# Kernel optimization log

Hardware: AMD Instinct MI355X
Metric: run time of the kernel (lower is better)

Reference implementation:

```python
import jax, jax.numpy as jnp
import numpy as np

D = 128   # node feature dim
C = 2     # classes
N = 50000 # nodes
E = 500000  # edges (before self-loops)
H1 = 2    # conv1 heads
NEG_SLOPE = 0.2
BN_EPS = 1e-5


def setup_inputs() -> dict:
    key = jax.random.key(0)
    ks = jax.random.split(key, 24)
    rn = lambda k, shape, s=0.05: jax.random.normal(k, shape, dtype=jnp.float32) * s
    inp = {
        'x': jax.random.normal(ks[0], (N, D), dtype=jnp.float32),
        'edge_index': jax.random.randint(ks[1], (2, E), 0, N, dtype=jnp.int64),
        # conv1: GATConv(D, D, heads=2, concat=True)
        'W1': rn(ks[2], (D, H1 * D)),
        'att_src1': rn(ks[3], (H1, D)),
        'att_dst1': rn(ks[4], (H1, D)),
        'bias1': jnp.zeros((H1 * D,), jnp.float32),
        # conv2: GATConv(2D, D, heads=1, concat=False)
        'W2': rn(ks[5], (2 * D, D)),
        'att_src2': rn(ks[6], (1, D)),
        'att_dst2': rn(ks[7], (1, D)),
        'bias2': jnp.zeros((D,), jnp.float32),
        # lin1 = MLP([3D, 96]) : Linear -> ReLU -> BatchNorm1d
        'Wl': rn(ks[8], (3 * D, 96)), 'bl': jnp.zeros((96,), jnp.float32),
        'gl': jnp.ones((96,), jnp.float32), 'betal': jnp.zeros((96,), jnp.float32),
        # mlp1 = MLP([96, 96, C]) : two (Linear -> ReLU -> BN) blocks
        'Wa': rn(ks[9], (96, 96)), 'ba': jnp.zeros((96,), jnp.float32),
        'ga': jnp.ones((96,), jnp.float32), 'betaa': jnp.zeros((96,), jnp.float32),
        'Wb': rn(ks[10], (96, C)), 'bb': jnp.zeros((C,), jnp.float32),
        'gb': jnp.ones((C,), jnp.float32), 'betab': jnp.zeros((C,), jnp.float32),
    }
    return inp


def gat_conv(x, src, dst, W, att_src, att_dst, bias, heads, out_dim, concat):
    # PyG GATConv: h = x W -> [N,H,F]; per-edge logit leakyrelu(a_s.h_src + a_d.h_dst);
    # segment softmax over edges grouped by destination; weighted scatter-sum.
    n = x.shape[0]
    h = (x @ W).reshape(n, heads, out_dim)
    a_src = jnp.einsum('nhd,hd->nh', h, att_src)  # [N,H]
    a_dst = jnp.einsum('nhd,hd->nh', h, att_dst)
    alpha = jax.nn.leaky_relu(a_src[src] + a_dst[dst], NEG_SLOPE)  # [Etot,H]
    m = jax.ops.segment_max(alpha, dst, num_segments=n)            # [N,H]
    e = jnp.exp(alpha - m[dst])
    s = jax.ops.segment_sum(e, dst, num_segments=n)
    w = e / (s[dst] + 1e-16)                                       # [Etot,H]
    out = jax.ops.segment_sum(h[src] * w[:, :, None], dst, num_segments=n)  # [N,H,F]
    out = out.reshape(n, heads * out_dim) if concat else out.mean(axis=1)
    return out + bias


def mlp_block(x, W, b, gamma, beta):
    # Linear -> ReLU -> BatchNorm1d (training-mode batch stats, biased var)
    y = jax.nn.relu(x @ W + b)
    mu = y.mean(axis=0)
    var = ((y - mu) ** 2).mean(axis=0)
    return gamma * (y - mu) / jnp.sqrt(var + BN_EPS) + beta


def reference(x, edge_index, W1, att_src1, att_dst1, bias1,
              W2, att_src2, att_dst2, bias2,
              Wl, bl, gl, betal, Wa, ba, ga, betaa, Wb, bb, gb, betab):
    n = x.shape[0]
    # PyG GATConv default add_self_loops=True
    loops = jnp.arange(n, dtype=edge_index.dtype)
    src = jnp.concatenate([edge_index[0], loops])
    dst = jnp.concatenate([edge_index[1], loops])
    x1 = gat_conv(x, src, dst, W1, att_src1, att_dst1, bias1, H1, D, True)    # [N,2D]
    x2 = gat_conv(x1, src, dst, W2, att_src2, att_dst2, bias2, 1, D, False)   # [N,D]
    h = jnp.concatenate([x1, x2], axis=1)                                      # [N,3D]
    h = mlp_block(h, Wl, bl, gl, betal)     # lin1
    h = mlp_block(h, Wa, ba, ga, betaa)     # mlp1 layer 1
    h = mlp_block(h, Wb, bb, gb, betab)     # mlp1 layer 2
    return h
```

## Files before the change

### kernel.cpp

```cpp
#include <hip/hip_runtime.h>
#include <hip/hip_bf16.h>
#include <cstdint>
#include <cstddef>

#define NNODES 50000
#define NEDGES 500000
#define ETOT   (NEDGES + NNODES)
#define MAXDEG 96

typedef __attribute__((ext_vector_type(8))) short short8;
typedef __attribute__((ext_vector_type(8))) unsigned short ushort8v;
typedef __attribute__((ext_vector_type(4))) float floatx4;
typedef __attribute__((ext_vector_type(4))) unsigned short ushort4v;

__device__ __forceinline__ unsigned short f2bf(float f) {
    union { __hip_bfloat16 h; unsigned short u; } cv;
    cv.h = __float2bfloat16(f);
    return cv.u;
}
__device__ __forceinline__ float bf2f(unsigned short u) {
    union { unsigned int i; float f; } cv;
    cv.i = ((unsigned int)u) << 16;
    return cv.f;
}

#define GBM 128
#define GBN 64
#define GBK 32

__global__ __launch_bounds__(256, 4) void gemm_mfma(
    const unsigned short* __restrict__ A, int lda,
    const unsigned short* __restrict__ Bt,
    float* __restrict__ C,
    unsigned short* __restrict__ Cb,
    const float* __restrict__ bias,
    float* __restrict__ colsum, float* __restrict__ colsq,
    const float* __restrict__ att_s, const float* __restrict__ att_d,
    float* __restrict__ as_out, float* __restrict__ ad_out, int Hheads,
    int M, int N, int K, int do_relu)
{
    __shared__ __attribute__((aligned(16))) unsigned short Alds[GBM * GBK];
    __shared__ __attribute__((aligned(16))) unsigned short Blds[GBN * GBK];
    __shared__ float scol[GBN], sqcol[GBN];

    int tid = threadIdx.x;
    int wave = tid >> 6, lane = tid & 63;
    int row0 = blockIdx.y * GBM;
    int col0 = blockIdx.x * GBN;
    int m = lane & 15, q = lane >> 4;

    floatx4 acc[2][4] = {};

    for (int k0 = 0; k0 < K; k0 += GBK) {
        #pragma unroll
        for (int i = 0; i < 2; ++i) {
            int c = tid + i * 256;
            int r = c >> 2, off = (c & 3) * 8;
            int gr = row0 + r;
            short8 v = {};
            if (gr < M) v = *(const short8*)(A + (size_t)gr * lda + k0 + off);
            *(short8*)(Alds + r * GBK + off) = v;
        }
        {
            int r = tid >> 2, off = (tid & 3) * 8;
            short8 v = *(const short8*)(Bt + (size_t)(col0 + r) * K + k0 + off);
            *(short8*)(Blds + r * GBK + off) = v;
        }
        __syncthreads();

        short8 a0 = *(const short8*)(Alds + (wave * 32 + m) * GBK + q * 8);
        short8 a1 = *(const short8*)(Alds + (wave * 32 + 16 + m) * GBK + q * 8);
        #pragma unroll
        for (int ct = 0; ct < 4; ++ct) {
            short8 b = *(const short8*)(Blds + (ct * 16 + m) * GBK + q * 8);
            acc[0][ct] = __builtin_amdgcn_mfma_f32_16x16x32_bf16(a0, b, acc[0][ct], 0, 0, 0);
            acc[1][ct] = __builtin_amdgcn_mfma_f32_16x16x32_bf16(a1, b, acc[1][ct], 0, 0, 0);
        }
        __syncthreads();
    }

    float ps[4] = {}, pq[4] = {};
    #pragma unroll
    for (int rt = 0; rt < 2; ++rt) {
        #pragma unroll
        for (int r = 0; r < 4; ++r) {
            int gr = row0 + wave * 32 + rt * 16 + q * 4 + r;
            float ds = 0.f, dd = 0.f;
            #pragma unroll
            for (int ct = 0; ct < 4; ++ct) {
                int gc = col0 + ct * 16 + m;
                float v = acc[rt][ct][r];
                if (gc < N) {
                    if (att_s != nullptr) { ds += v * att_s[gc]; dd += v * att_d[gc]; }
                    float vb = v;
                    if (bias != nullptr) vb += bias[gc];
                    if (do_relu) vb = fmaxf(vb, 0.f);
                    if (gr < M) {
                        if (C  != nullptr) C[(size_t)gr * N + gc] = vb;
                        if (Cb != nullptr) Cb[(size_t)gr * N + gc] = f2bf(vb);
                        ps[ct] += vb; pq[ct] += vb * vb;
                    }
                }
            }
            if (att_s != nullptr) {
                #pragma unroll
                for (int off = 1; off < 16; off <<= 1) {
                    ds += __shfl_xor(ds, off);
                    dd += __shfl_xor(dd, off);
                }
                if (m == 0 && gr < M) {
                    int head = col0 >> 7;
                    atomicAdd(&as_out[gr * Hheads + head], ds);
                    atomicAdd(&ad_out[gr * Hheads + head], dd);
                }
            }
        }
    }
    if (colsum != nullptr) {
        if (tid < GBN) { scol[tid] = 0.f; sqcol[tid] = 0.f; }
        __syncthreads();
        #pragma unroll
        for (int ct = 0; ct < 4; ++ct) {
            atomicAdd(&scol[ct * 16 + m], ps[ct]);
            atomicAdd(&sqcol[ct * 16 + m], pq[ct]);
        }
        __syncthreads();
        if (tid < GBN) {
            int gc = col0 + tid;
            if (gc < N) {
                atomicAdd(&colsum[gc], scol[tid]);
                atomicAdd(&colsq[gc], sqcol[tid]);
            }
        }
    }
}

__global__ void cast_x_k(const float* __restrict__ x, unsigned short* __restrict__ xb, int total4) {
    int i = blockIdx.x * blockDim.x + threadIdx.x;
    if (i >= total4) return;
    const float4 v = ((const float4*)x)[i];
    ushort4v o;
    o.x = f2bf(v.x); o.y = f2bf(v.y); o.z = f2bf(v.z); o.w = f2bf(v.w);
    ((ushort4v*)xb)[i] = o;
}

__global__ void cast_weights(const float* __restrict__ W1, const float* __restrict__ W2,
                             const float* __restrict__ Wl,
                             unsigned short* __restrict__ W1t, unsigned short* __restrict__ W2t,
                             unsigned short* __restrict__ Wlt) {
    int i = blockIdx.x * 256 + threadIdx.x;
    if (i < 32768) {
        int n = i >> 7, k = i & 127;
        W1t[i] = f2bf(W1[k * 256 + n]);
    } else if (i < 65536) {
        int j = i - 32768;
        int n = j >> 8, k = j & 255;
        W2t[j] = f2bf(W2[k * 128 + n]);
    } else if (i < 114688) {
        int j = i - 65536;
        int n = j / 384, k = j % 384;
        Wlt[j] = (n < 96) ? f2bf(Wl[(size_t)k * 96 + n]) : (unsigned short)0;
    }
}

__global__ void bnfold_a(const float* __restrict__ csum, const float* __restrict__ csq,
                         const float* __restrict__ gamma, const float* __restrict__ beta,
                         const float* __restrict__ Wa, const float* __restrict__ ba,
                         unsigned short* __restrict__ Wat2, float* __restrict__ ba_f) {
    __shared__ float scl[96], shf[96];
    int tid = threadIdx.x;
    if (tid < 96) {
        float mu  = csum[tid] / (float)NNODES;
        float var = csq[tid] / (float)NNODES - mu * mu;
        if (var < 0.f) var = 0.f;
        float sc = gamma[tid] * rsqrtf(var + 1e-5f);
        scl[tid] = sc; shf[tid] = beta[tid] - mu * sc;
    }
    __syncthreads();
    for (int idx = tid; idx < 128 * 96; idx += 256) {
        int n = idx / 96, k = idx % 96;
        Wat2[idx] = (n < 96) ? f2bf(scl[k] * Wa[k * 96 + n]) : (unsigned short)0;
    }
    if (tid < 96) {
        float s = ba[tid];
        for (int k = 0; k < 96; ++k) s += shf[k] * Wa[k * 96 + tid];
        ba_f[tid] = s;
    }
}

__global__ void bnfold_b(const float* __restrict__ csum, const float* __restrict__ csq,
                         const float* __restrict__ gamma, const float* __restrict__ beta,
                         const float* __restrict__ Wb, const float* __restrict__ bb,
                         unsigned short* __restrict__ Wbt, float* __restrict__ bb_f) {
    __shared__ float scl[96], shf[96];
    int tid = threadIdx.x;
    if (tid < 96) {
        float mu  = csum[tid] / (float)NNODES;
        float var = csq[tid] / (float)NNODES - mu * mu;
        if (var < 0.f) var = 0.f;
        float sc = gamma[tid] * rsqrtf(var + 1e-5f);
        scl[tid] = sc; shf[tid] = beta[tid] - mu * sc;
    }
    __syncthreads();
    for (int idx = tid; idx < 64 * 96; idx += 256) {
        int n = idx / 96, k = idx % 96;
        Wbt[idx] = (n < 2) ? f2bf(scl[k] * Wb[k * 2 + n]) : (unsigned short)0;
    }
    if (tid < 2) {
        float s = bb[tid];
        for (int k = 0; k < 96; ++k) s += shf[k] * Wb[k * 2 + tid];
        bb_f[tid] = s;
    }
}

__global__ void bn_fin_apply(const float* __restrict__ csum, const float* __restrict__ csq,
                             const float* __restrict__ gamma, const float* __restrict__ beta,
                             float* __restrict__ y, int total) {
    int i = blockIdx.x * blockDim.x + threadIdx.x;
    if (i >= total) return;
    int j = i & 1;
    float mu  = csum[j] / (float)NNODES;
    float var = csq[j] / (float)NNODES - mu * mu;
    if (var < 0.f) var = 0.f;
    float sc = gamma[j] * rsqrtf(var + 1e-5f);
    float sh = beta[j] - mu * sc;
    y[i] = y[i] * sc + sh;
}

__device__ __forceinline__ void edge_src_dst(const int* ei, int e, int& src, int& dst) {
    if (e < NEDGES) { src = ei[e]; dst = ei[NEDGES + e]; }
    else { src = e - NEDGES; dst = src; }
}

__global__ __launch_bounds__(256) void csr_count(const int* __restrict__ ei, int* __restrict__ cnt) {
    int e = blockIdx.x * blockDim.x + threadIdx.x;
    if (e >= ETOT) return;
    int src, dst; edge_src_dst(ei, e, src, dst); (void)src;
    atomicAdd(&cnt[dst], 1);
}

#define SCAN_CH 1024
#define SCAN_NB ((NNODES + SCAN_CH - 1) / SCAN_CH)

__global__ __launch_bounds__(256) void scan1(const int* __restrict__ cnt, int* __restrict__ part) {
    int t = threadIdx.x;
    int base = blockIdx.x * SCAN_CH + t * 4;
    int4 v = {0, 0, 0, 0};
    if (base + 3 < NNODES) v = *(const int4*)(cnt + base);
    else {
        if (base + 0 < NNODES) v.x = cnt[base + 0];
        if (base + 1 < NNODES) v.y = cnt[base + 1];
        if (base + 2 < NNODES) v.z = cnt[base + 2];
        if (base + 3 < NNODES) v.w = cnt[base + 3];
    }
    int s = v.x + v.y + v.z + v.w;
    __shared__ int sm[256];
    sm[t] = s;
    __syncthreads();
    for (int off = 128; off > 0; off >>= 1) {
        if (t < off) sm[t] += sm[t + off];
        __syncthreads();
    }
    if (t == 0) part[blockIdx.x] = sm[0];
}

__global__ void scan2(int* __restrict__ part, int* __restrict__ rowstart) {
    int lane = threadIdx.x;
    int v = (lane < SCAN_NB) ? part[lane] : 0;
    #pragma unroll
    for (int off = 1; off < 64; off <<= 1) {
        int t = __shfl_up(v, off);
        if (lane >= off) v += t;
    }
    int ex = __shfl_up(v, 1);
    if (lane == 0) ex = 0;
    if (lane < SCAN_NB) part[lane] = ex;
    if (lane == 0) rowstart[NNODES] = ETOT;
}

__global__ __launch_bounds__(256) void scan3(const int* __restrict__ cnt, const int* __restrict__ part,
                                             int* __restrict__ rowstart, int* __restrict__ cursor) {
    int t = threadIdx.x;
    int base = blockIdx.x * SCAN_CH + t * 4;
    int4 v = {0, 0, 0, 0};
    if (base + 3 < NNODES) v = *(const int4*)(cnt + base);
    else {
        if (base + 0 < NNODES) v.x = cnt[base + 0];
        if (base + 1 < NNODES) v.y = cnt[base + 1];
        if (base + 2 < NNODES) v.z = cnt[base + 2];
        if (base + 3 < NNODES) v.w = cnt[base + 3];
    }
    int s = v.x + v.y + v.z + v.w;
    __shared__ int sm[2][256];
    sm[0][t] = s;
    __syncthreads();
    int cur = 0;
    #pragma unroll
    for (int off = 1; off < 256; off <<= 1) {
        int nxt = cur ^ 1;
        int val = sm[cur][t];
        if (t >= off) val += sm[cur][t - off];
        sm[nxt][t] = val;
        __syncthreads();
        cur = nxt;
    }
    int p = sm[cur][t] - s + part[blockIdx.x];
    if (base + 0 < NNODES) { rowstart[base + 0] = p; cursor[base + 0] = p; } p += v.x;
    if (base + 1 < NNODES) { rowstart[base + 1] = p; cursor[base + 1] = p; } p += v.y;
    if (base + 2 < NNODES) { rowstart[base + 2] = p; cursor[base + 2] = p; } p += v.z;
    if (base + 3 < NNODES) { rowstart[base + 3] = p; cursor[base + 3] = p; }
}

__global__ __launch_bounds__(256) void csr_fill(const int* __restrict__ ei,
                                                int* __restrict__ cursor,
                                                int* __restrict__ esrc) {
    int e = blockIdx.x * blockDim.x + threadIdx.x;
    if (e >= ETOT) return;
    int src, dst; edge_src_dst(ei, e, src, dst);
    int pos = atomicAdd(&cursor[dst], 1);
    esrc[pos] = src;
}

__global__ __launch_bounds__(256) void gat_gather_h2(
    const int* __restrict__ rowstart, const int* __restrict__ esrc,
    const unsigned short* __restrict__ hb, const float* __restrict__ a_src,
    const float* __restrict__ a_dst, const float* __restrict__ bias,
    unsigned short* __restrict__ xcat)
{
    __shared__ float wl[4][2][MAXDEG];
    __shared__ int   esl[4][MAXDEG];
    int wave = threadIdx.x >> 6;
    int n = (blockIdx.x * blockDim.x + threadIdx.x) >> 6;
    int lane = threadIdx.x & 63;
    if (n >= NNODES) return;
    int beg = rowstart[n], end = rowstart[n + 1];
    int deg = end - beg;
    float ad0 = a_dst[n * 2], ad1 = a_dst[n * 2 + 1];

    float m0 = -1e30f, m1 = -1e30f;
    for (int idx = lane; idx < deg; idx += 64) {
        int s = esrc[beg + idx];
        float l0 = a_src[s * 2] + ad0;     l0 = l0 >= 0.f ? l0 : 0.2f * l0;
        float l1 = a_src[s * 2 + 1] + ad1; l1 = l1 >= 0.f ? l1 : 0.2f * l1;
        m0 = fmaxf(m0, l0); m1 = fmaxf(m1, l1);
        if (idx < MAXDEG) { wl[wave][0][idx] = l0; wl[wave][1][idx] = l1; esl[wave][idx] = s; }
    }
    #pragma unroll
    for (int off = 1; off < 64; off <<= 1) {
        m0 = fmaxf(m0, __shfl_xor(m0, off));
        m1 = fmaxf(m1, __shfl_xor(m1, off));
    }
    float s0 = 0.f, s1 = 0.f;
    for (int idx = lane; idx < deg; idx += 64) {
        float l0, l1;
        if (idx < MAXDEG) { l0 = wl[wave][0][idx]; l1 = wl[wave][1][idx]; }
        else {
            int s = esrc[beg + idx];
            l0 = a_src[s * 2] + ad0;     l0 = l0 >= 0.f ? l0 : 0.2f * l0;
            l1 = a_src[s * 2 + 1] + ad1; l1 = l1 >= 0.f ? l1 : 0.2f * l1;
        }
        float e0 = __expf(l0 - m0), e1 = __expf(l1 - m1);
        s0 += e0; s1 += e1;
        if (idx < MAXDEG) { wl[wave][0][idx] = e0; wl[wave][1][idx] = e1; }
    }
    #pragma unroll
    for (int off = 1; off < 64; off <<= 1) {
        s0 += __shfl_xor(s0, off);
        s1 += __shfl_xor(s1, off);
    }

    int g  = lane >> 5;
    int sl = lane & 31;
    int head = sl >> 4;
    float mh   = head ? m1 : m0;
    float invh = head ? 1.f / (s1 + 1e-16f) : 1.f / (s0 + 1e-16f);
    float adh  = head ? ad1 : ad0;

    float acc[8] = {}, acc2[8] = {};
    for (int idx = g; idx < deg; idx += 4) {
        int sA; float wA;
        if (idx < MAXDEG) { sA = esl[wave][idx]; wA = wl[wave][head][idx] * invh; }
        else {
            sA = esrc[beg + idx];
            float l = a_src[sA * 2 + head] + adh; l = l >= 0.f ? l : 0.2f * l;
            wA = __expf(l - mh) * invh;
        }
        const ushort8v hvA = *(const ushort8v*)(hb + (size_t)sA * 256 + sl * 8);
        int i2 = idx + 2;
        if (i2 < deg) {
            int sB; float wB;
            if (i2 < MAXDEG) { sB = esl[wave][i2]; wB = wl[wave][head][i2] * invh; }
            else {
                sB = esrc[beg + i2];
                float l = a_src[sB * 2 + head] + adh; l = l >= 0.f ? l : 0.2f * l;
                wB = __expf(l - mh) * invh;
            }
            const ushort8v hvB = *(const ushort8v*)(hb + (size_t)sB * 256 + sl * 8);
            #pragma unroll
            for (int j = 0; j < 8; ++j) acc2[j] += wB * bf2f(hvB[j]);
        }
        #pragma unroll
        for (int j = 0; j < 8; ++j) acc[j] += wA * bf2f(hvA[j]);
    }
    #pragma unroll
    for (int j = 0; j < 8; ++j) acc[j] += acc2[j];
    #pragma unroll
    for (int j = 0; j < 8; ++j) acc[j] += __shfl_xor(acc[j], 32);
    if (g == 0) {
        ushort8v o;
        #pragma unroll
        for (int j = 0; j < 8; ++j) o[j] = f2bf(acc[j] + bias[sl * 8 + j]);
        *(ushort8v*)(xcat + (size_t)n * 384 + sl * 8) = o;
    }
}

__global__ __launch_bounds__(256) void gat_gather_h1(
    const int* __restrict__ rowstart, const int* __restrict__ esrc,
    const unsigned short* __restrict__ hb, const float* __restrict__ a_src,
    const float* __restrict__ a_dst, const float* __restrict__ bias,
    unsigned short* __restrict__ xcat)
{
    __shared__ float wl[4][MAXDEG];
    __shared__ int   esl[4][MAXDEG];
    int wave = threadIdx.x >> 6;
    int n = (blockIdx.x * blockDim.x + threadIdx.x) >> 6;
    int lane = threadIdx.x & 63;
    if (n >= NNODES) return;
    int beg = rowstart[n], end = rowstart[n + 1];
    int deg = end - beg;
    float ad0 = a_dst[n];

    float m0 = -1e30f;
    for (int idx = lane; idx < deg; idx += 64) {
        int s = esrc[beg + idx];
        float l0 = a_src[s] + ad0; l0 = l0 >= 0.f ? l0 : 0.2f * l0;
        m0 = fmaxf(m0, l0);
        if (idx < MAXDEG) { wl[wave][idx] = l0; esl[wave][idx] = s; }
    }
    #pragma unroll
    for (int off = 1; off < 64; off <<= 1) m0 = fmaxf(m0, __shfl_xor(m0, off));
    float s0 = 0.f;
    for (int idx = lane; idx < deg; idx += 64) {
        float l0;
        if (idx < MAXDEG) l0 = wl[wave][idx];
        else {
            int s = esrc[beg + idx];
            l0 = a_src[s] + ad0; l0 = l0 >= 0.f ? l0 : 0.2f * l0;
        }
        float e0 = __expf(l0 - m0);
        s0 += e0;
        if (idx < MAXDEG) wl[wave][idx] = e0;
    }
    #pragma unroll
    for (int off = 1; off < 64; off <<= 1) s0 += __shfl_xor(s0, off);
    float inv0 = 1.f / (s0 + 1e-16f);

    int g  = lane >> 4;
    int sl = lane & 15;

    float acc[8] = {}, acc2[8] = {};
    for (int idx = g; idx < deg; idx += 8) {
        int sA; float wA;
        if (idx < MAXDEG) { sA = esl[wave][idx]; wA = wl[wave][idx] * inv0; }
        else {
            sA = esrc[beg + idx];
            float l = a_src[sA] + ad0; l = l >= 0.f ? l : 0.2f * l;
            wA = __expf(l - m0) * inv0;
        }
        const ushort8v hvA = *(const ushort8v*)(hb + (size_t)sA * 128 + sl * 8);
        int i2 = idx + 4;
        if (i2 < deg) {
            int sB; float wB;
            if (i2 < MAXDEG) { sB = esl[wave][i2]; wB = wl[wave][i2] * inv0; }
            else {
                sB = esrc[beg + i2];
                float l = a_src[sB] + ad0; l = l >= 0.f ? l : 0.2f * l;
                wB = __expf(l - m0) * inv0;
            }
            const ushort8v hvB = *(const ushort8v*)(hb + (size_t)sB * 128 + sl * 8);
            #pragma unroll
            for (int j = 0; j < 8; ++j) acc2[j] += wB * bf2f(hvB[j]);
        }
        #pragma unroll
        for (int j = 0; j < 8; ++j) acc[j] += wA * bf2f(hvA[j]);
    }
    #pragma unroll
    for (int j = 0; j < 8; ++j) acc[j] += acc2[j];
    #pragma unroll
    for (int j = 0; j < 8; ++j) acc[j] += __shfl_xor(acc[j], 16);
    #pragma unroll
    for (int j = 0; j < 8; ++j) acc[j] += __shfl_xor(acc[j], 32);
    if (g == 0) {
        ushort8v o;
        #pragma unroll
        for (int j = 0; j < 8; ++j) o[j] = f2bf(acc[j] + bias[sl * 8 + j]);
        *(ushort8v*)(xcat + (size_t)n * 384 + 256 + sl * 8) = o;
    }
}

extern "C" void kernel_launch(void* const* d_in, const int* in_sizes, int n_in,
                              void* d_out, int out_size, void* d_ws, size_t ws_size,
                              hipStream_t stream) {
    const float* x        = (const float*)d_in[0];
    const int*   ei       = (const int*)d_in[1];
    const float* W1       = (const float*)d_in[2];
    const float* att_src1 = (const float*)d_in[3];
    const float* att_dst1 = (const float*)d_in[4];
    const float* bias1    = (const float*)d_in[5];
    const float* W2       = (const float*)d_in[6];
    const float* att_src2 = (const float*)d_in[7];
    const float* att_dst2 = (const float*)d_in[8];
    const float* bias2    = (const float*)d_in[9];
    const float* Wl       = (const float*)d_in[10];
    const float* bl       = (const float*)d_in[11];
    const float* gl       = (const float*)d_in[12];
    const float* betal    = (const float*)d_in[13];
    const float* Wa       = (const float*)d_in[14];
    const float* ba       = (const float*)d_in[15];
    const float* ga       = (const float*)d_in[16];
    const float* betaa    = (const float*)d_in[17];
    const float* Wb       = (const float*)d_in[18];
    const float* bb       = (const float*)d_in[19];
    const float* gb       = (const float*)d_in[20];
    const float* betab    = (const float*)d_in[21];
    float* out = (float*)d_out;
    char* ws = (char*)d_ws;

    const int N = NNODES;

    const size_t offY2b  = 0;
    const size_t offXcat = 19200000;
    const size_t offXb   = 57600000;
    const size_t offY1b  = 70400000;
    const size_t offHb1  = 80000000;
    const size_t offW1t  = 105600000;
    const size_t offW2t  = 105665536;
    const size_t offWlt  = 105731072;
    const size_t offWat2 = 105829376;
    const size_t offWbt  = 105853952;
    const size_t offBaf  = 105866240;
    const size_t offBbf  = 105866640;
    const size_t offRow  = 106000000;
    const size_t offCur  = 106200128;
    const size_t offEsrc = 106400832;
    const size_t offPart = 108700000;
    const size_t offAs1  = 108800000;
    const size_t offAd1  = 109200000;
    const size_t offAs2  = 109600000;
    const size_t offAd2  = 109800000;
    const size_t offSt   = 110000000;

    unsigned short* y2b  = (unsigned short*)(ws + offY2b);
    unsigned short* xcat = (unsigned short*)(ws + offXcat);
    unsigned short* xb   = (unsigned short*)(ws + offXb);
    unsigned short* hb2  = (unsigned short*)(ws + offXb);
    unsigned short* y1b  = (unsigned short*)(ws + offY1b);
    unsigned short* hb1  = (unsigned short*)(ws + offHb1);
    unsigned short* W1t  = (unsigned short*)(ws + offW1t);
    unsigned short* W2t  = (unsigned short*)(ws + offW2t);
    unsigned short* Wlt  = (unsigned short*)(ws + offWlt);
    unsigned short* Wat2 = (unsigned short*)(ws + offWat2);
    unsigned short* Wbt  = (unsigned short*)(ws + offWbt);
    float* ba_f = (float*)(ws + offBaf);
    float* bb_f = (float*)(ws + offBbf);
    int* rowst  = (int*)(ws + offRow);
    int* cursor = (int*)(ws + offCur);
    int* esrc   = (int*)(ws + offEsrc);
    int* part   = (int*)(ws + offPart);
    float* as1  = (float*)(ws + offAs1);
    float* ad1  = (float*)(ws + offAd1);
    float* as2  = (float*)(ws + offAs2);
    float* ad2  = (float*)(ws + offAd2);

    float* csum_l = (float*)(ws + offSt + 0);
    float* csq_l  = (float*)(ws + offSt + 512);
    float* csum_a = (float*)(ws + offSt + 2048);
    float* csq_a  = (float*)(ws + offSt + 2560);
    float* csum_b = (float*)(ws + offSt + 4096);
    float* csq_b  = (float*)(ws + offSt + 4608);

    hipMemsetAsync(ws + offRow, 0, (NNODES + 1) * sizeof(int), stream);
    hipMemsetAsync(ws + offAs1, 0, (offSt + 6144) - offAs1, stream);

    dim3 blk(256);
    int edgeBlocks  = (ETOT + 255) / 256;
    int waveBlocksN = (N + 3) / 4;

    cast_x_k<<<(N * 128 / 4 + 255) / 256, blk, 0, stream>>>(x, xb, N * 128 / 4);
    cast_weights<<<(114688 + 255) / 256, blk, 0, stream>>>(W1, W2, Wl, W1t, W2t, Wlt);

    csr_count<<<edgeBlocks, blk, 0, stream>>>(ei, rowst);
    scan1<<<SCAN_NB, blk, 0, stream>>>(rowst, part);
    scan2<<<1, 64, 0, stream>>>(part, rowst);
    scan3<<<SCAN_NB, blk, 0, stream>>>(rowst, part, rowst, cursor);
    csr_fill<<<edgeBlocks, blk, 0, stream>>>(ei, cursor, esrc);

    gemm_mfma<<<dim3(4, (N + GBM - 1) / GBM), blk, 0, stream>>>(
        xb, 128, W1t, nullptr, hb1, nullptr, nullptr, nullptr,
        att_src1, att_dst1, as1, ad1, 2, N, 256, 128, 0);
    gat_gather_h2<<<waveBlocksN, blk, 0, stream>>>(rowst, esrc, hb1, as1, ad1, bias1, xcat);

    gemm_mfma<<<dim3(2, (N + GBM - 1) / GBM), blk, 0, stream>>>(
        xcat, 384, W2t, nullptr, hb2, nullptr, nullptr, nullptr,
        att_src2, att_dst2, as2, ad2, 1, N, 128, 256, 0);
    gat_gather_h1<<<waveBlocksN, blk, 0, stream>>>(rowst, esrc, hb2, as2, ad2, bias2, xcat);

    gemm_mfma<<<dim3(2, (N + GBM - 1) / GBM), blk, 0, stream>>>(
        xcat, 384, Wlt, nullptr, y1b, bl, csum_l, csq_l,
        nullptr, nullptr, nullptr, nullptr, 0, N, 96, 384, 1);
    bnfold_a<<<1, 256, 0, stream>>>(csum_l, csq_l, gl, betal, Wa, ba, Wat2, ba_f);

    gemm_mfma<<<dim3(2, (N + GBM - 1) / GBM), blk, 0, stream>>>(
        y1b, 96, Wat2, nullptr, y2b, ba_f, csum_a, csq_a,
        nullptr, nullptr, nullptr, nullptr, 0, N, 96, 96, 1);
    bnfold_b<<<1, 256, 0, stream>>>(csum_a, csq_a, ga, betaa, Wb, bb, Wbt, bb_f);

    gemm_mfma<<<dim3(1, (N + GBM - 1) / GBM), blk, 0, stream>>>(
        y2b, 96, Wbt, out, nullptr, bb_f, csum_b, csq_b,
        nullptr, nullptr, nullptr, nullptr, 0, N, 2, 96, 1);

    bn_fin_apply<<<(N * 2 + 255) / 256, blk, 0, stream>>>(csum_b, csq_b, gb, betab, out, N * 2);
}
```

Baseline: 394.6 us.

## Split GAT edge-softmax into separate per-edge weight kernel before gather

Result: slower. 407.6 us (+3.3%).

```diff
diff --git a/kernel.cpp b/kernel.cpp
--- a/kernel.cpp
+++ b/kernel.cpp
@@ -6,7 +6,6 @@
 #define NNODES 50000
 #define NEDGES 500000
 #define ETOT   (NEDGES + NNODES)
-#define MAXDEG 96
 
 typedef __attribute__((ext_vector_type(8))) short short8;
 typedef __attribute__((ext_vector_type(8))) unsigned short ushort8v;
@@ -321,80 +320,111 @@
     esrc[pos] = src;
 }
 
+__global__ __launch_bounds__(256) void edge_w_h2(
+    const int* __restrict__ rowstart, const int* __restrict__ esrc,
+    const float* __restrict__ a_src, const float* __restrict__ a_dst,
+    float2* __restrict__ wedge)
+{
+    int g  = threadIdx.x >> 4;
+    int sl = threadIdx.x & 15;
+    int n = blockIdx.x * 16 + g;
+    if (n >= NNODES) return;
+    int beg = rowstart[n], deg = rowstart[n + 1] - beg;
+    float ad0 = a_dst[n * 2], ad1 = a_dst[n * 2 + 1];
+
+    float m0 = -1e30f, m1 = -1e30f;
+    for (int i = sl; i < deg; i += 16) {
+        int s = esrc[beg + i];
+        float l0 = a_src[s * 2] + ad0;     l0 = l0 >= 0.f ? l0 : 0.2f * l0;
+        float l1 = a_src[s * 2 + 1] + ad1; l1 = l1 >= 0.f ? l1 : 0.2f * l1;
+        m0 = fmaxf(m0, l0); m1 = fmaxf(m1, l1);
+    }
+    #pragma unroll
+    for (int off = 1; off < 16; off <<= 1) {
+        m0 = fmaxf(m0, __shfl_xor(m0, off));
+        m1 = fmaxf(m1, __shfl_xor(m1, off));
+    }
+    float s0 = 0.f, s1 = 0.f;
+    for (int i = sl; i < deg; i += 16) {
+        int s = esrc[beg + i];
+        float l0 = a_src[s * 2] + ad0;     l0 = l0 >= 0.f ? l0 : 0.2f * l0;
+        float l1 = a_src[s * 2 + 1] + ad1; l1 = l1 >= 0.f ? l1 : 0.2f * l1;
+        float e0 = __expf(l0 - m0), e1 = __expf(l1 - m1);
+        s0 += e0; s1 += e1;
+        float2 w; w.x = e0; w.y = e1;
+        wedge[beg + i] = w;
+    }
+    #pragma unroll
+    for (int off = 1; off < 16; off <<= 1) {
+        s0 += __shfl_xor(s0, off);
+        s1 += __shfl_xor(s1, off);
+    }
+    float inv0 = 1.f / (s0 + 1e-16f), inv1 = 1.f / (s1 + 1e-16f);
+    for (int i = sl; i < deg; i += 16) {
+        float2 w = wedge[beg + i];
+        w.x *= inv0; w.y *= inv1;
+        wedge[beg + i] = w;
+    }
+}
+
+__global__ __launch_bounds__(256) void edge_w_h1(
+    const int* __restrict__ rowstart, const int* __restrict__ esrc,
+    const float* __restrict__ a_src, const float* __restrict__ a_dst,
+    float* __restrict__ wedge)
+{
+    int g  = threadIdx.x >> 4;
+    int sl = threadIdx.x & 15;
+    int n = blockIdx.x * 16 + g;
+    if (n >= NNODES) return;
+    int beg = rowstart[n], deg = rowstart[n + 1] - beg;
+    float ad0 = a_dst[n];
+
+    float m0 = -1e30f;
+    for (int i = sl; i < deg; i += 16) {
+        int s = esrc[beg + i];
+        float l0 = a_src[s] + ad0; l0 = l0 >= 0.f ? l0 : 0.2f * l0;
+        m0 = fmaxf(m0, l0);
+    }
+    #pragma unroll
+    for (int off = 1; off < 16; off <<= 1) m0 = fmaxf(m0, __shfl_xor(m0, off));
+    float s0 = 0.f;
+    for (int i = sl; i < deg; i += 16) {
+        int s = esrc[beg + i];
+        float l0 = a_src[s] + ad0; l0 = l0 >= 0.f ? l0 : 0.2f * l0;
+        float e0 = __expf(l0 - m0);
+        s0 += e0;
+        wedge[beg + i] = e0;
+    }
+    #pragma unroll
+    for (int off = 1; off < 16; off <<= 1) s0 += __shfl_xor(s0, off);
+    float inv0 = 1.f / (s0 + 1e-16f);
+    for (int i = sl; i < deg; i += 16) wedge[beg + i] *= inv0;
+}
+
 __global__ __launch_bounds__(256) void gat_gather_h2(
     const int* __restrict__ rowstart, const int* __restrict__ esrc,
-    const unsigned short* __restrict__ hb, const float* __restrict__ a_src,
-    const float* __restrict__ a_dst, const float* __restrict__ bias,
-    unsigned short* __restrict__ xcat)
+    const unsigned short* __restrict__ hb, const float2* __restrict__ wedge,
+    const float* __restrict__ bias, unsigned short* __restrict__ xcat)
 {
-    __shared__ float wl[4][2][MAXDEG];
-    __shared__ int   esl[4][MAXDEG];
-    int wave = threadIdx.x >> 6;
     int n = (blockIdx.x * blockDim.x + threadIdx.x) >> 6;
     int lane = threadIdx.x & 63;
     if (n >= NNODES) return;
-    int beg = rowstart[n], end = rowstart[n + 1];
-    int deg = end - beg;
-    float ad0 = a_dst[n * 2], ad1 = a_dst[n * 2 + 1];
-
-    float m0 = -1e30f, m1 = -1e30f;
-    for (int idx = lane; idx < deg; idx += 64) {
-        int s = esrc[beg + idx];
-        float l0 = a_src[s * 2] + ad0;     l0 = l0 >= 0.f ? l0 : 0.2f * l0;
-        float l1 = a_src[s * 2 + 1] + ad1; l1 = l1 >= 0.f ? l1 : 0.2f * l1;
-        m0 = fmaxf(m0, l0); m1 = fmaxf(m1, l1);
-        if (idx < MAXDEG) { wl[wave][0][idx] = l0; wl[wave][1][idx] = l1; esl[wave][idx] = s; }
-    }
-    #pragma unroll
-    for (int off = 1; off < 64; off <<= 1) {
-        m0 = fmaxf(m0, __shfl_xor(m0, off));
-        m1 = fmaxf(m1, __shfl_xor(m1, off));
-    }
-    float s0 = 0.f, s1 = 0.f;
-    for (int idx = lane; idx < deg; idx += 64) {
-        float l0, l1;
-        if (idx < MAXDEG) { l0 = wl[wave][0][idx]; l1 = wl[wave][1][idx]; }
-        else {
-            int s = esrc[beg + idx];
-            l0 = a_src[s * 2] + ad0;     l0 = l0 >= 0.f ? l0 : 0.2f * l0;
-            l1 = a_src[s * 2 + 1] + ad1; l1 = l1 >= 0.f ? l1 : 0.2f * l1;
-        }
-        float e0 = __expf(l0 - m0), e1 = __expf(l1 - m1);
-        s0 += e0; s1 += e1;
-        if (idx < MAXDEG) { wl[wave][0][idx] = e0; wl[wave][1][idx] = e1; }
-    }
-    #pragma unroll
-    for (int off = 1; off < 64; off <<= 1) {
-        s0 += __shfl_xor(s0, off);
-        s1 += __shfl_xor(s1, off);
-    }
-
-    int g  = lane >> 5;
-    int sl = lane & 31;
-    int head = sl >> 4;
-    float mh   = head ? m1 : m0;
-    float invh = head ? 1.f / (s1 + 1e-16f) : 1.f / (s0 + 1e-16f);
-    float adh  = head ? ad1 : ad0;
+    int beg = rowstart[n], deg = rowstart[n + 1] - beg;
+    const int* es = esrc + beg;
+    const float2* we = wedge + beg;
+    int g = lane >> 5, sl = lane & 31, head = sl >> 4;
 
     float acc[8] = {}, acc2[8] = {};
     for (int idx = g; idx < deg; idx += 4) {
-        int sA; float wA;
-        if (idx < MAXDEG) { sA = esl[wave][idx]; wA = wl[wave][head][idx] * invh; }
-        else {
-            sA = esrc[beg + idx];
-            float l = a_src[sA * 2 + head] + adh; l = l >= 0.f ? l : 0.2f * l;
-            wA = __expf(l - mh) * invh;
-        }
+        int sA = es[idx];
+        float2 wv = we[idx];
+        float wA = head ? wv.y : wv.x;
         const ushort8v hvA = *(const ushort8v*)(hb + (size_t)sA * 256 + sl * 8);
         int i2 = idx + 2;
         if (i2 < deg) {
-            int sB; float wB;
-            if (i2 < MAXDEG) { sB = esl[wave][i2]; wB = wl[wave][head][i2] * invh; }
-            else {
-                sB = esrc[beg + i2];
-                float l = a_src[sB * 2 + head] + adh; l = l >= 0.f ? l : 0.2f * l;
-                wB = __expf(l - mh) * invh;
-            }
+            int sB = es[i2];
+            float2 wv2 = we[i2];
+            float wB = head ? wv2.y : wv2.x;
             const ushort8v hvB = *(const ushort8v*)(hb + (size_t)sB * 256 + sl * 8);
             #pragma unroll
             for (int j = 0; j < 8; ++j) acc2[j] += wB * bf2f(hvB[j]);
@@ -416,67 +446,26 @@
 
 __global__ __launch_bounds__(256) void gat_gather_h1(
     const int* __restrict__ rowstart, const int* __restrict__ esrc,
-    const unsigned short* __restrict__ hb, const float* __restrict__ a_src,
-    const float* __restrict__ a_dst, const float* __restrict__ bias,
-    unsigned short* __restrict__ xcat)
+    const unsigned short* __restrict__ hb, const float* __restrict__ wedge,
+    const float* __restrict__ bias, unsigned short* __restrict__ xcat)
 {
-    __shared__ float wl[4][MAXDEG];
-    __shared__ int   esl[4][MAXDEG];
-    int wave = threadIdx.x >> 6;
     int n = (blockIdx.x * blockDim.x + threadIdx.x) >> 6;
     int lane = threadIdx.x & 63;
     if (n >= NNODES) return;
-    int beg = rowstart[n], end = rowstart[n + 1];
-    int deg = end - beg;
-    float ad0 = a_dst[n];
-
-    float m0 = -1e30f;
-    for (int idx = lane; idx < deg; idx += 64) {
-        int s = esrc[beg + idx];
-        float l0 = a_src[s] + ad0; l0 = l0 >= 0.f ? l0 : 0.2f * l0;
-        m0 = fmaxf(m0, l0);
-        if (idx < MAXDEG) { wl[wave][idx] = l0; esl[wave][idx] = s; }
-    }
-    #pragma unroll
-    for (int off = 1; off < 64; off <<= 1) m0 = fmaxf(m0, __shfl_xor(m0, off));
-    float s0 = 0.f;
-    for (int idx = lane; idx < deg; idx += 64) {
-        float l0;
-        if (idx < MAXDEG) l0 = wl[wave][idx];
-        else {
-            int s = esrc[beg + idx];
-            l0 = a_src[s] + ad0; l0 = l0 >= 0.f ? l0 : 0.2f * l0;
-        }
-        float e0 = __expf(l0 - m0);
-        s0 += e0;
-        if (idx < MAXDEG) wl[wave][idx] = e0;
-    }
-    #pragma unroll
-    for (int off = 1; off < 64; off <<= 1) s0 += __shfl_xor(s0, off);
-    float inv0 = 1.f / (s0 + 1e-16f);
-
-    int g  = lane >> 4;
-    int sl = lane & 15;
+    int beg = rowstart[n], deg = rowstart[n + 1] - beg;
+    const int* es = esrc + beg;
+    const float* we = wedge + beg;
+    int g = lane >> 4, sl = lane & 15;
 
     float acc[8] = {}, acc2[8] = {};
     for (int idx = g; idx < deg; idx += 8) {
-        int sA; float wA;
-        if (idx < MAXDEG) { sA = esl[wave][idx]; wA = wl[wave][idx] * inv0; }
-        else {
-            sA = esrc[beg + idx];
-            float l = a_src[sA] + ad0; l = l >= 0.f ? l : 0.2f * l;
-            wA = __expf(l - m0) * inv0;
-        }
+        int sA = es[idx];
+        float wA = we[idx];
         const ushort8v hvA = *(const ushort8v*)(hb + (size_t)sA * 128 + sl * 8);
         int i2 = idx + 4;
         if (i2 < deg) {
-            int sB; float wB;
-            if (i2 < MAXDEG) { sB = esl[wave][i2]; wB = wl[wave][i2] * inv0; }
-            else {
-                sB = esrc[beg + i2];
-                float l = a_src[sB] + ad0; l = l >= 0.f ? l : 0.2f * l;
-                wB = __expf(l - m0) * inv0;
-            }
+            int sB = es[i2];
+            float wB = we[i2];
             const ushort8v hvB = *(const ushort8v*)(hb + (size_t)sB * 128 + sl * 8);
             #pragma unroll
             for (int j = 0; j < 8; ++j) acc2[j] += wB * bf2f(hvB[j]);
@@ -528,6 +517,7 @@
 
     const int N = NNODES;
 
+    const size_t offWedge= 0;
     const size_t offY2b  = 0;
     const size_t offXcat = 19200000;
     const size_t offXb   = 57600000;
@@ -550,6 +540,8 @@
     const size_t offAd2  = 109800000;
     const size_t offSt   = 110000000;
 
+    float2* wedge2 = (float2*)(ws + offWedge);
+    float*  wedge1 = (float*)(ws + offWedge);
     unsigned short* y2b  = (unsigned short*)(ws + offY2b);
     unsigned short* xcat = (unsigned short*)(ws + offXcat);
     unsigned short* xb   = (unsigned short*)(ws + offXb);
@@ -585,6 +577,7 @@
     dim3 blk(256);
     int edgeBlocks  = (ETOT + 255) / 256;
     int waveBlocksN = (N + 3) / 4;
+    int grpBlocksN  = (N + 15) / 16;
 
     cast_x_k<<<(N * 128 / 4 + 255) / 256, blk, 0, stream>>>(x, xb, N * 128 / 4);
     cast_weights<<<(114688 + 255) / 256, blk, 0, stream>>>(W1, W2, Wl, W1t, W2t, Wlt);
@@ -598,12 +591,14 @@
     gemm_mfma<<<dim3(4, (N + GBM - 1) / GBM), blk, 0, stream>>>(
         xb, 128, W1t, nullptr, hb1, nullptr, nullptr, nullptr,
         att_src1, att_dst1, as1, ad1, 2, N, 256, 128, 0);
-    gat_gather_h2<<<waveBlocksN, blk, 0, stream>>>(rowst, esrc, hb1, as1, ad1, bias1, xcat);
+    edge_w_h2<<<grpBlocksN, blk, 0, stream>>>(rowst, esrc, as1, ad1, wedge2);
+    gat_gather_h2<<<waveBlocksN, blk, 0, stream>>>(rowst, esrc, hb1, wedge2, bias1, xcat);
 
     gemm_mfma<<<dim3(2, (N + GBM - 1) / GBM), blk, 0, stream>>>(
         xcat, 384, W2t, nullptr, hb2, nullptr, nullptr, nullptr,
         att_src2, att_dst2, as2, ad2, 1, N, 128, 256, 0);
-    gat_gather_h1<<<waveBlocksN, blk, 0, stream>>>(rowst, esrc, hb2, as2, ad2, bias2, xcat);
+    edge_w_h1<<<grpBlocksN, blk, 0, stream>>>(rowst, esrc, as2, ad2, wedge1);
+    gat_gather_h1<<<waveBlocksN, blk, 0, stream>>>(rowst, esrc, hb2, wedge1, bias2, xcat);
 
     gemm_mfma<<<dim3(2, (N + GBM - 1) / GBM), blk, 0, stream>>>(
         xcat, 384, Wlt, nullptr, y1b, bl, csum_l, csq_l,
```
